# Optimization experiments

Hardware: AMD Instinct MI355X
Metric: run time of the kernel (lower is better)

The kernel has to match this reference:

```python
import jax, jax.numpy as jnp
import numpy as np

FP8_MAX = 448.0  # torch.finfo(float8_e4m3fn).max

def _fp8_round(v):
    # round-to-nearest fp8 e4m3fn, back to f32 (simulated quantization)
    return v.astype(jnp.float8_e4m3fn).astype(jnp.float32)

def setup_inputs() -> dict:
    key = jax.random.key(0)
    k_x, k_w, k_b = jax.random.split(key, 3)
    M, K, N = 8, 8192, 8192
    x = jax.random.normal(k_x, (M, K), dtype=jnp.float32)
    w = jax.random.normal(k_w, (K, N), dtype=jnp.float32) * 0.02
    # per-output-column weight quantization (amax-to-scale)
    w_amax = jnp.max(jnp.abs(w), axis=0)                      # [N]
    w_scale = jnp.where(w_amax > 0, FP8_MAX / w_amax, 1.0)    # [N]
    weight_fp8_t = _fp8_round(w * w_scale[None, :])           # [K, N] fp8 values in f32
    weight_scale_inv = (1.0 / w_scale).astype(jnp.float32)    # [N]
    bias = jax.random.normal(k_b, (N,), dtype=jnp.float32) * 0.01
    return {"x": x, "weight_fp8_t": weight_fp8_t,
            "weight_scale_inv": weight_scale_inv, "bias": bias}

def reference(x, weight_fp8_t, weight_scale_inv, bias):
    # dynamic per-row activation quantization: amax -> scale
    amax = jnp.max(jnp.abs(x), axis=-1)                       # [M]
    x_scale = jnp.where(amax > 0, FP8_MAX / amax, 1.0)        # [M]
    x_fp8 = _fp8_round(x * x_scale[:, None])                  # [M, K]
    # scaled matmul: acc * x_scale_inv * weight_scale_inv (per row / per col)
    acc = jnp.einsum('mk,kn->mn', x_fp8, weight_fp8_t)        # [M, N]
    y = acc * (1.0 / x_scale)[:, None] * weight_scale_inv[None, :]
    return y + bias[None, :]
```

## Files before the change

kernel.cpp:

```cpp
#include <hip/hip_runtime.h>
#include <stdint.h>

#define MM 8
#define KK 8192
#define NN 8192
#define KC 256
#define KSPLIT (KK / KC)
#define G 8
#define FP8MAXV 448.0f

typedef float f32x4 __attribute__((ext_vector_type(4)));
typedef float f32x2 __attribute__((ext_vector_type(2)));

#define XQT_OFF 64
#define PART_OFF (XQT_OFF + KK * MM)

__device__ __forceinline__ float fp8_e4m3_round(float v) {
    uint32_t u = __float_as_uint(v);
    uint32_t mag = u & 0x7fffffffu;
    if (mag >= 0x3C800000u) {
        uint32_t lsb = (u >> 20) & 1u;
        uint32_t r = u + 0x0007FFFFu + lsb;
        r &= 0xFFF00000u;
        return __uint_as_float(r);
    }
    return rintf(v * 512.0f) * (1.0f / 512.0f);
}

__global__ __launch_bounds__(256) void prep_kernel(const float* __restrict__ x,
                                                   float* __restrict__ ws) {
    const int m = blockIdx.x;
    const int tid = threadIdx.x;
    const float* row = x + (size_t)m * KK;

    float amax = 0.0f;
    for (int k = tid * 4; k < KK; k += 256 * 4) {
        f32x4 v = *(const f32x4*)(row + k);
        amax = fmaxf(amax, fmaxf(fmaxf(fabsf(v.x), fabsf(v.y)),
                                 fmaxf(fabsf(v.z), fabsf(v.w))));
    }
#pragma unroll
    for (int off = 32; off >= 1; off >>= 1)
        amax = fmaxf(amax, __shfl_xor(amax, off, 64));

    __shared__ float sred[4];
    __shared__ float sscale;
    if ((tid & 63) == 0) sred[tid >> 6] = amax;
    __syncthreads();
    if (tid == 0) {
        float a = fmaxf(fmaxf(sred[0], sred[1]), fmaxf(sred[2], sred[3]));
        float scale = (a > 0.0f) ? (FP8MAXV / a) : 1.0f;
        sscale = scale;
        ws[m] = 1.0f / scale;
    }
    __syncthreads();
    const float scale = sscale;

    float* xqT = ws + XQT_OFF;
    for (int k = tid; k < KK; k += 256)
        xqT[(size_t)k * MM + m] = fp8_e4m3_round(row[k] * scale);
}

__global__ __launch_bounds__(256, 2) void gemm_partial(const float* __restrict__ W,
                                                       const float* __restrict__ wsinv,
                                                       const float* __restrict__ ws,
                                                       float* __restrict__ part) {
    const int tid = threadIdx.x;
    const int n2  = (blockIdx.x * 256 + tid) * 2;
    const int c   = blockIdx.y;
    const int k0  = c * KC;

    const float* __restrict__ Wp = W + (size_t)k0 * NN + n2;
    const float* __restrict__ xq = ws + XQT_OFF + (size_t)k0 * MM;

    f32x2 acc[MM];
#pragma unroll
    for (int m = 0; m < MM; ++m) acc[m] = (f32x2)0.0f;

    f32x2 wA[G], wB[G];

    auto loadg = [&](f32x2 (&buf)[G], int gbase) {
#pragma unroll
        for (int j = 0; j < G; ++j)
            buf[j] = *(const f32x2*)(Wp + (size_t)(gbase + j) * NN);
    };
    auto compute = [&](f32x2 (&buf)[G], int gbase) {
#pragma unroll
        for (int j = 0; j < G; ++j) {
            const float* a = xq + (size_t)(gbase + j) * MM;
            f32x2 w = buf[j];
            acc[0] += w * a[0];
            acc[1] += w * a[1];
            acc[2] += w * a[2];
            acc[3] += w * a[3];
            acc[4] += w * a[4];
            acc[5] += w * a[5];
            acc[6] += w * a[6];
            acc[7] += w * a[7];
        }
    };

    loadg(wA, 0 * G);
    loadg(wB, 1 * G);
    int g = 0;
    for (; g + 2 < KC / G; g += 2) {
        compute(wA, (g + 0) * G);
        loadg(wA, (g + 2) * G);
        compute(wB, (g + 1) * G);
        loadg(wB, (g + 3) * G);
    }
    compute(wA, (g + 0) * G);
    compute(wB, (g + 1) * G);

    const f32x2 wsn = *(const f32x2*)(wsinv + n2);
    float* p = part + ((size_t)c * MM) * NN + n2;
#pragma unroll
    for (int m = 0; m < MM; ++m)
        *(f32x2*)(p + (size_t)m * NN) = acc[m] * (ws[m] * wsn);
}

__global__ __launch_bounds__(256) void reduce_kernel(const float* __restrict__ part,
                                                     const float* __restrict__ bias,
                                                     float* __restrict__ out) {
    const int idx = blockIdx.x * 256 + threadIdx.x;
    float s = bias[idx & (NN - 1)];
#pragma unroll
    for (int c = 0; c < KSPLIT; ++c)
        s += part[(size_t)c * MM * NN + idx];
    out[idx] = s;
}

__global__ __launch_bounds__(256) void init_kernel(const float* __restrict__ bias,
                                                   float* __restrict__ out) {
    int idx = blockIdx.x * 256 + threadIdx.x;
    out[idx] = bias[idx & (NN - 1)];
}

__global__ __launch_bounds__(256, 2) void gemm_atomic(const float* __restrict__ W,
                                                      const float* __restrict__ wsinv,
                                                      const float* __restrict__ ws,
                                                      float* __restrict__ out) {
    const int tid = threadIdx.x;
    const int n2  = (blockIdx.x * 256 + tid) * 2;
    const int k0  = blockIdx.y * KC;

    const float* __restrict__ Wp = W + (size_t)k0 * NN + n2;
    const float* __restrict__ xq = ws + XQT_OFF + (size_t)k0 * MM;

    f32x2 acc[MM];
#pragma unroll
    for (int m = 0; m < MM; ++m) acc[m] = (f32x2)0.0f;

    for (int k = 0; k < KC; ++k) {
        f32x2 w = *(const f32x2*)(Wp + (size_t)k * NN);
        const float* a = xq + (size_t)k * MM;
#pragma unroll
        for (int m = 0; m < MM; ++m) acc[m] += w * a[m];
    }

    const f32x2 wsn = *(const f32x2*)(wsinv + n2);
#pragma unroll
    for (int m = 0; m < MM; ++m) {
        f32x2 r = acc[m] * (ws[m] * wsn);
        unsafeAtomicAdd(out + (size_t)m * NN + n2 + 0, r.x);
        unsafeAtomicAdd(out + (size_t)m * NN + n2 + 1, r.y);
    }
}

extern "C" void kernel_launch(void* const* d_in, const int* in_sizes, int n_in,
                              void* d_out, int out_size, void* d_ws, size_t ws_size,
                              hipStream_t stream) {
    const float* x     = (const float*)d_in[0];
    const float* W     = (const float*)d_in[1];
    const float* wsinv = (const float*)d_in[2];
    const float* bias  = (const float*)d_in[3];
    float* out = (float*)d_out;
    float* ws  = (float*)d_ws;

    const size_t need = (size_t)(PART_OFF + (size_t)KSPLIT * MM * NN) * sizeof(float);

    prep_kernel<<<MM, 256, 0, stream>>>(x, ws);

    if (ws_size >= need) {
        float* part = ws + PART_OFF;
        gemm_partial<<<dim3(NN / 512, KSPLIT), 256, 0, stream>>>(W, wsinv, ws, part);
        reduce_kernel<<<(MM * NN) / 256, 256, 0, stream>>>(part, bias, out);
    } else {
        init_kernel<<<(MM * NN) / 256, 256, 0, stream>>>(bias, out);
        gemm_atomic<<<dim3(NN / 512, KSPLIT), 256, 0, stream>>>(W, wsinv, ws, out);
    }
}
```

Baseline: 77.64 us.

## Widen GEMM to four columns per thread, stage activations in LDS, halve K chunk

Each thread in the split-K GEMM now owns four output columns and loads the weight matrix as 128-bit vectors instead of 64-bit pairs. The per-chunk quantized activations are staged once into shared memory and read back as vectors, and the per-row scales are hoisted to registers. The K chunk shrinks from 256 to 128, which keeps the block count the same, but doubles the number of partial sums the reduce kernel has to write and read. The goal is better memory-load efficiency on the dominant weight stream. The costs are extra partial-sum traffic, a larger workspace requirement, and possible register pressure from the wider accumulators.

```diff
diff --git a/kernel.cpp b/kernel.cpp
--- a/kernel.cpp
+++ b/kernel.cpp
@@ -4,13 +4,12 @@
 #define MM 8
 #define KK 8192
 #define NN 8192
-#define KC 256
+#define KC 128
 #define KSPLIT (KK / KC)
-#define G 8
+#define G 4
 #define FP8MAXV 448.0f
 
 typedef float f32x4 __attribute__((ext_vector_type(4)));
-typedef float f32x2 __attribute__((ext_vector_type(2)));
 
 #define XQT_OFF 64
 #define PART_OFF (XQT_OFF + KK * MM)
@@ -66,37 +65,44 @@
                                                        const float* __restrict__ ws,
                                                        float* __restrict__ part) {
     const int tid = threadIdx.x;
-    const int n2  = (blockIdx.x * 256 + tid) * 2;
+    const int n4  = (blockIdx.x * 256 + tid) * 4;
     const int c   = blockIdx.y;
     const int k0  = c * KC;
 
-    const float* __restrict__ Wp = W + (size_t)k0 * NN + n2;
-    const float* __restrict__ xq = ws + XQT_OFF + (size_t)k0 * MM;
-
-    f32x2 acc[MM];
-#pragma unroll
-    for (int m = 0; m < MM; ++m) acc[m] = (f32x2)0.0f;
-
-    f32x2 wA[G], wB[G];
-
-    auto loadg = [&](f32x2 (&buf)[G], int gbase) {
+    __shared__ f32x4 sxq[KC * MM / 4];
+    sxq[tid] = ((const f32x4*)(ws + XQT_OFF + (size_t)k0 * MM))[tid];
+
+    const f32x4 xs0 = *(const f32x4*)(ws);
+    const f32x4 xs1 = *(const f32x4*)(ws + 4);
+    const f32x4 wsn = *(const f32x4*)(wsinv + n4);
+    __syncthreads();
+
+    f32x4 acc[MM];
+#pragma unroll
+    for (int m = 0; m < MM; ++m) acc[m] = (f32x4)0.0f;
+
+    const float* __restrict__ Wp = W + (size_t)k0 * NN + n4;
+
+    f32x4 wA[G], wB[G];
+    auto loadg = [&](f32x4 (&buf)[G], int kbase) {
 #pragma unroll
         for (int j = 0; j < G; ++j)
-            buf[j] = *(const f32x2*)(Wp + (size_t)(gbase + j) * NN);
+            buf[j] = *(const f32x4*)(Wp + (size_t)(kbase + j) * NN);
     };
-    auto compute = [&](f32x2 (&buf)[G], int gbase) {
+    auto compute = [&](f32x4 (&buf)[G], int kbase) {
 #pragma unroll
         for (int j = 0; j < G; ++j) {
-            const float* a = xq + (size_t)(gbase + j) * MM;
-            f32x2 w = buf[j];
-            acc[0] += w * a[0];
-            acc[1] += w * a[1];
-            acc[2] += w * a[2];
-            acc[3] += w * a[3];
-            acc[4] += w * a[4];
-            acc[5] += w * a[5];
-            acc[6] += w * a[6];
-            acc[7] += w * a[7];
+            f32x4 a0 = sxq[(kbase + j) * 2 + 0];
+            f32x4 a1 = sxq[(kbase + j) * 2 + 1];
+            f32x4 w  = buf[j];
+            acc[0] += w * a0.x;
+            acc[1] += w * a0.y;
+            acc[2] += w * a0.z;
+            acc[3] += w * a0.w;
+            acc[4] += w * a1.x;
+            acc[5] += w * a1.y;
+            acc[6] += w * a1.z;
+            acc[7] += w * a1.w;
         }
     };
 
@@ -112,11 +118,11 @@
     compute(wA, (g + 0) * G);
     compute(wB, (g + 1) * G);
 
-    const f32x2 wsn = *(const f32x2*)(wsinv + n2);
-    float* p = part + ((size_t)c * MM) * NN + n2;
+    float xsa[MM] = {xs0.x, xs0.y, xs0.z, xs0.w, xs1.x, xs1.y, xs1.z, xs1.w};
+    float* p = part + ((size_t)c * MM) * NN + n4;
 #pragma unroll
     for (int m = 0; m < MM; ++m)
-        *(f32x2*)(p + (size_t)m * NN) = acc[m] * (ws[m] * wsn);
+        *(f32x4*)(p + (size_t)m * NN) = acc[m] * (xsa[m] * wsn);
 }
 
 __global__ __launch_bounds__(256) void reduce_kernel(const float* __restrict__ part,
@@ -124,9 +130,9 @@
                                                      float* __restrict__ out) {
     const int idx = blockIdx.x * 256 + threadIdx.x;
     float s = bias[idx & (NN - 1)];
-#pragma unroll
+#pragma unroll 16
     for (int c = 0; c < KSPLIT; ++c)
-        s += part[(size_t)c * MM * NN + idx];
+        s += part[(size_t)c * (MM * NN) + idx];
     out[idx] = s;
 }
 
@@ -141,29 +147,40 @@
                                                       const float* __restrict__ ws,
                                                       float* __restrict__ out) {
     const int tid = threadIdx.x;
-    const int n2  = (blockIdx.x * 256 + tid) * 2;
+    const int n4  = (blockIdx.x * 256 + tid) * 4;
     const int k0  = blockIdx.y * KC;
 
-    const float* __restrict__ Wp = W + (size_t)k0 * NN + n2;
-    const float* __restrict__ xq = ws + XQT_OFF + (size_t)k0 * MM;
-
-    f32x2 acc[MM];
-#pragma unroll
-    for (int m = 0; m < MM; ++m) acc[m] = (f32x2)0.0f;
-
+    __shared__ f32x4 sxq[KC * MM / 4];
+    sxq[tid] = ((const f32x4*)(ws + XQT_OFF + (size_t)k0 * MM))[tid];
+    const f32x4 xs0 = *(const f32x4*)(ws);
+    const f32x4 xs1 = *(const f32x4*)(ws + 4);
+    const f32x4 wsn = *(const f32x4*)(wsinv + n4);
+    __syncthreads();
+
+    f32x4 acc[MM];
+#pragma unroll
+    for (int m = 0; m < MM; ++m) acc[m] = (f32x4)0.0f;
+
+    const float* __restrict__ Wp = W + (size_t)k0 * NN + n4;
     for (int k = 0; k < KC; ++k) {
-        f32x2 w = *(const f32x2*)(Wp + (size_t)k * NN);
-        const float* a = xq + (size_t)k * MM;
-#pragma unroll
-        for (int m = 0; m < MM; ++m) acc[m] += w * a[m];
-    }
-
-    const f32x2 wsn = *(const f32x2*)(wsinv + n2);
+        f32x4 w  = *(const f32x4*)(Wp + (size_t)k * NN);
+        f32x4 a0 = sxq[k * 2 + 0];
+        f32x4 a1 = sxq[k * 2 + 1];
+        acc[0] += w * a0.x;  acc[1] += w * a0.y;
+        acc[2] += w * a0.z;  acc[3] += w * a0.w;
+        acc[4] += w * a1.x;  acc[5] += w * a1.y;
+        acc[6] += w * a1.z;  acc[7] += w * a1.w;
+    }
+
+    float xsa[MM] = {xs0.x, xs0.y, xs0.z, xs0.w, xs1.x, xs1.y, xs1.z, xs1.w};
 #pragma unroll
     for (int m = 0; m < MM; ++m) {
-        f32x2 r = acc[m] * (ws[m] * wsn);
-        unsafeAtomicAdd(out + (size_t)m * NN + n2 + 0, r.x);
-        unsafeAtomicAdd(out + (size_t)m * NN + n2 + 1, r.y);
+        f32x4 r = acc[m] * (xsa[m] * wsn);
+        float* o = out + (size_t)m * NN + n4;
+        unsafeAtomicAdd(o + 0, r.x);
+        unsafeAtomicAdd(o + 1, r.y);
+        unsafeAtomicAdd(o + 2, r.z);
+        unsafeAtomicAdd(o + 3, r.w);
     }
 }
 
@@ -183,10 +200,10 @@
 
     if (ws_size >= need) {
         float* part = ws + PART_OFF;
-        gemm_partial<<<dim3(NN / 512, KSPLIT), 256, 0, stream>>>(W, wsinv, ws, part);
+        gemm_partial<<<dim3(NN / 1024, KSPLIT), 256, 0, stream>>>(W, wsinv, ws, part);
         reduce_kernel<<<(MM * NN) / 256, 256, 0, stream>>>(part, bias, out);
     } else {
         init_kernel<<<(MM * NN) / 256, 256, 0, stream>>>(bias, out);
-        gemm_atomic<<<dim3(NN / 512, KSPLIT), 256, 0, stream>>>(W, wsinv, ws, out);
-    }
-}
+        gemm_atomic<<<dim3(NN / 1024, KSPLIT), 256, 0, stream>>>(W, wsinv, ws, out);
+    }
+}
```

Result: faster. 72.14 us (-7.1%).
